# Kernel tuning notes

Hardware: AMD Instinct MI355X
Metric: run time of the kernel (lower is better)

Reference implementation:

```python
import jax, jax.numpy as jnp
import numpy as np

N_LAYER = 4
N_HEAD = 8
N_EMBD = 512
HEAD_SIZE = N_EMBD // N_HEAD
VOCAB = 32000
BLOCK = 2048
WINDOW = 64
N_GLOBAL = 16
N_RANDOM = 16
B = 2
T = 2048


def setup_inputs() -> dict:
    key = jax.random.key(0)
    ks = jax.random.split(key, 24)
    s = 0.02
    inp = {
        "tok_emb": jax.random.normal(ks[0], (VOCAB, N_EMBD), jnp.float32) * s,
        "pos_emb": jax.random.normal(ks[1], (BLOCK, N_EMBD), jnp.float32) * s,
        "Wq": jax.random.normal(ks[2], (N_LAYER, N_HEAD, N_EMBD, HEAD_SIZE), jnp.float32) * s,
        "Wk": jax.random.normal(ks[3], (N_LAYER, N_HEAD, N_EMBD, HEAD_SIZE), jnp.float32) * s,
        "Wv": jax.random.normal(ks[4], (N_LAYER, N_HEAD, N_EMBD, HEAD_SIZE), jnp.float32) * s,
        "Wproj": jax.random.normal(ks[5], (N_LAYER, N_EMBD, N_EMBD), jnp.float32) * s,
        "bproj": jnp.zeros((N_LAYER, N_EMBD), jnp.float32),
        "ln1_g": jnp.ones((N_LAYER, N_EMBD), jnp.float32),
        "ln1_b": jnp.zeros((N_LAYER, N_EMBD), jnp.float32),
        "ln2_g": jnp.ones((N_LAYER, N_EMBD), jnp.float32),
        "ln2_b": jnp.zeros((N_LAYER, N_EMBD), jnp.float32),
        "W1": jax.random.normal(ks[6], (N_LAYER, N_EMBD, 4 * N_EMBD), jnp.float32) * s,
        "b1": jnp.zeros((N_LAYER, 4 * N_EMBD), jnp.float32),
        "W2": jax.random.normal(ks[7], (N_LAYER, 4 * N_EMBD, N_EMBD), jnp.float32) * s,
        "b2": jnp.zeros((N_LAYER, N_EMBD), jnp.float32),
        "lnf_g": jnp.ones((N_EMBD,), jnp.float32),
        "lnf_b": jnp.zeros((N_EMBD,), jnp.float32),
        "Wout": jax.random.normal(ks[8], (N_EMBD, VOCAB), jnp.float32) * s,
        "bout": jnp.zeros((VOCAB,), jnp.float32),
        "input_tokens": jax.random.randint(ks[9], (B, T), 0, VOCAB, jnp.int32),
        "random_cols": jax.random.randint(ks[10], (N_LAYER, N_HEAD, T, N_RANDOM), 0, T, jnp.int32),
    }
    return inp


def _layernorm(x, g, b):
    mu = jnp.mean(x, axis=-1, keepdims=True)
    var = jnp.var(x, axis=-1, keepdims=True)
    return (x - mu) * jax.lax.rsqrt(var + 1e-5) * g + b


def _static_masks(t):
    rows = jnp.arange(t)[:, None]
    cols = jnp.arange(t)[None, :]
    causal = rows >= cols
    local = (cols >= rows - WINDOW + 1) & (cols <= rows)
    glob = (rows < N_GLOBAL) | (cols < N_GLOBAL)
    return local | glob, causal  # base [T,T], causal [T,T]


def _random_mask(rc):  # rc: [H, T, R] -> [H, T, T] bool
    h, t, r = rc.shape
    m = jnp.zeros((h, t, t), dtype=bool)
    hi = jnp.arange(h)[:, None, None]
    ri = jnp.arange(t)[None, :, None]
    return m.at[hi, ri, rc].set(True)


def _forward(tok_emb, pos_emb, Wq, Wk, Wv, Wproj, bproj, ln1_g, ln1_b, ln2_g, ln2_b,
             W1, b1, W2, b2, lnf_g, lnf_b, Wout, bout, input_tokens, random_cols):
    b, t = input_tokens.shape
    x = tok_emb[input_tokens] + pos_emb[:t]  # [B,T,C]
    base, causal = _static_masks(t)
    scale = HEAD_SIZE ** -0.5
    neg_inf = jnp.finfo(x.dtype).min
    for l in range(N_LAYER):
        xn = _layernorm(x, ln1_g[l], ln1_b[l])
        q = jnp.einsum('btc,hcd->bhtd', xn, Wq[l])
        k = jnp.einsum('btc,hcd->bhtd', xn, Wk[l])
        v = jnp.einsum('btc,hcd->bhtd', xn, Wv[l])
        w = jnp.einsum('bhtd,bhsd->bhts', q, k) * scale  # [B,H,T,T]
        final = (base[None] | _random_mask(random_cols[l])) & causal[None]  # [H,T,T]
        w = jnp.where(final[None], w, neg_inf)
        w = jax.nn.softmax(w, axis=-1)
        attn = jnp.einsum('bhts,bhsd->bhtd', w, v)  # [B,H,T,hs]
        attn = attn.transpose(0, 2, 1, 3).reshape(b, t, N_EMBD)
        x = x + attn @ Wproj[l] + bproj[l]
        xn = _layernorm(x, ln2_g[l], ln2_b[l])
        h = jax.nn.relu(xn @ W1[l] + b1[l])
        x = x + h @ W2[l] + b2[l]
    x = _layernorm(x, lnf_g, lnf_b)
    return x @ Wout + bout  # logits [B,T,V]


def reference(tok_emb, pos_emb, Wq, Wk, Wv, Wproj, bproj, ln1_g, ln1_b, ln2_g, ln2_b,
              W1, b1, W2, b2, lnf_g, lnf_b, Wout, bout, input_tokens, random_cols):
    return _forward(tok_emb, pos_emb, Wq, Wk, Wv, Wproj, bproj, ln1_g, ln1_b, ln2_g, ln2_b,
                    W1, b1, W2, b2, lnf_g, lnf_b, Wout, bout, input_tokens, random_cols)
```

## Files before the change

kernel.cpp:

```cpp
#include <hip/hip_runtime.h>
#include <hip/hip_bf16.h>

#define NLAYER 4
#define NHEAD 8
#define CEMB 512
#define HS 64
#define VOCAB_N 32000
#define SEQT 2048
#define BATCH_N 2
#define MROWS (BATCH_N * SEQT)
#define WIN 64
#define NGLOB 16
#define NRAND 16
#define QB 16

typedef __attribute__((ext_vector_type(8))) __bf16 bf16x8;
typedef __attribute__((ext_vector_type(4))) float f32x4;
typedef __attribute__((ext_vector_type(8))) unsigned short u16x8;

__device__ __forceinline__ unsigned short f2bf(float f) {
    unsigned u = __float_as_uint(f);
    u += 0x7fffu + ((u >> 16) & 1u);
    return (unsigned short)(u >> 16);
}
__device__ __forceinline__ float bf2f(unsigned short v) {
    return __uint_as_float((unsigned)v << 16);
}

__device__ __forceinline__ void stage16(const unsigned short* g, unsigned short* l) {
    __builtin_amdgcn_global_load_lds(
        (const __attribute__((address_space(1))) void*)g,
        (__attribute__((address_space(3))) void*)l, 16, 0, 0);
}

__global__ __launch_bounds__(256) void transpose_all_kernel(
    const float* __restrict__ Wq, const float* __restrict__ Wk,
    const float* __restrict__ Wv, const float* __restrict__ Wproj,
    const float* __restrict__ W1, const float* __restrict__ W2,
    const float* __restrict__ Wout,
    unsigned short* __restrict__ wqkvT, unsigned short* __restrict__ wprojT,
    unsigned short* __restrict__ w1T, unsigned short* __restrict__ w2T,
    unsigned short* __restrict__ woutT)
{
    __shared__ float tle[64][65];
    const int bid = blockIdx.x;
    const float* src; unsigned short* dst; int Ks, Ns, k0, n0;
    if (bid < 768) {
        const int tile = bid & 7, rest = bid >> 3;
        const int l = rest / 24, r2 = rest % 24;
        const int sel = r2 >> 3, h = r2 & 7;
        const float* W = (sel == 0) ? Wq : (sel == 1) ? Wk : Wv;
        src = W + (size_t)(l * 8 + h) * 512 * 64;
        dst = wqkvT + ((size_t)l * 1536 + sel * 512 + h * 64) * 512;
        Ks = 512; Ns = 64; k0 = tile * 64; n0 = 0;
    } else if (bid < 1024) {
        const int idx = bid - 768, l = idx >> 6, t6 = idx & 63;
        src = Wproj + (size_t)l * 512 * 512;
        dst = wprojT + (size_t)l * 512 * 512;
        Ks = 512; Ns = 512; k0 = (t6 >> 3) * 64; n0 = (t6 & 7) * 64;
    } else if (bid < 2048) {
        const int idx = bid - 1024, l = idx >> 8, t8 = idx & 255;
        src = W1 + (size_t)l * 512 * 2048;
        dst = w1T + (size_t)l * 2048 * 512;
        Ks = 512; Ns = 2048; k0 = (t8 >> 5) * 64; n0 = (t8 & 31) * 64;
    } else if (bid < 3072) {
        const int idx = bid - 2048, l = idx >> 8, t8 = idx & 255;
        src = W2 + (size_t)l * 2048 * 512;
        dst = w2T + (size_t)l * 512 * 2048;
        Ks = 2048; Ns = 512; k0 = (t8 >> 3) * 64; n0 = (t8 & 7) * 64;
    } else {
        const int idx = bid - 3072;
        src = Wout; dst = woutT;
        Ks = 512; Ns = 32000; k0 = (idx / 500) * 64; n0 = (idx % 500) * 64;
    }
    const int tid = threadIdx.x;
    #pragma unroll
    for (int i = 0; i < 16; ++i) {
        const int idx = tid + i * 256;
        const int r = idx >> 6, c = idx & 63;
        tle[r][c] = src[(size_t)(k0 + r) * Ns + n0 + c];
    }
    __syncthreads();
    #pragma unroll
    for (int i = 0; i < 16; ++i) {
        const int idx = tid + i * 256;
        const int c = idx >> 6, r = idx & 63;
        dst[(size_t)(n0 + c) * Ks + k0 + r] = f2bf(tle[r][c]);
    }
}

__global__ __launch_bounds__(256) void embed_kernel(
    const float* __restrict__ tok_emb, const float* __restrict__ pos_emb,
    const int* __restrict__ toks, float* __restrict__ x)
{
    int i = blockIdx.x * 256 + threadIdx.x;
    int m = i >> 7;
    int c = (i & 127) << 2;
    int tok = toks[m];
    const float4 a = *(const float4*)&tok_emb[(size_t)tok * CEMB + c];
    const float4 p = *(const float4*)&pos_emb[(size_t)(m & (SEQT - 1)) * CEMB + c];
    float4 o;
    o.x = a.x + p.x; o.y = a.y + p.y; o.z = a.z + p.z; o.w = a.w + p.w;
    *(float4*)&x[(size_t)m * CEMB + c] = o;
}

__global__ __launch_bounds__(256) void ln_kernel(
    const float* __restrict__ x, const float* __restrict__ g,
    const float* __restrict__ b, unsigned short* __restrict__ out)
{
    const int wave = threadIdx.x >> 6, lane = threadIdx.x & 63;
    const int m = blockIdx.x * 4 + wave;
    const float* row = x + (size_t)m * CEMB;
    const float4 v0 = *(const float4*)&row[lane * 8];
    const float4 v1 = *(const float4*)&row[lane * 8 + 4];
    float s  = v0.x + v0.y + v0.z + v0.w + v1.x + v1.y + v1.z + v1.w;
    float s2 = v0.x*v0.x + v0.y*v0.y + v0.z*v0.z + v0.w*v0.w
             + v1.x*v1.x + v1.y*v1.y + v1.z*v1.z + v1.w*v1.w;
    #pragma unroll
    for (int off = 32; off > 0; off >>= 1) {
        s  += __shfl_xor(s, off);
        s2 += __shfl_xor(s2, off);
    }
    const float mu  = s * (1.f / CEMB);
    const float var = s2 * (1.f / CEMB) - mu * mu;
    const float rs  = rsqrtf(var + 1e-5f);
    const float vals[8] = {v0.x, v0.y, v0.z, v0.w, v1.x, v1.y, v1.z, v1.w};
    u16x8 o;
    #pragma unroll
    for (int j = 0; j < 8; ++j)
        o[j] = f2bf((vals[j] - mu) * rs * g[lane * 8 + j] + b[lane * 8 + j]);
    *(u16x8*)&out[(size_t)m * CEMB + lane * 8] = o;
}

template<int MODE, int NF, int SWZ>
__global__ __launch_bounds__(256) void gemm_kernel(
    const unsigned short* __restrict__ A, const unsigned short* __restrict__ Bt,
    const float* __restrict__ bias, const float* resid, void* outp,
    int M, int N, int K)
{
    __shared__ unsigned short sa[3][128 * 32];
    __shared__ unsigned short sb[3][NF * 32 * 32];
    const int tid = threadIdx.x;
    const int lane = tid & 63;
    const int wave = tid >> 6;
    const int wr = wave >> 1, wc = wave & 1;

    int bx = blockIdx.x, by = blockIdx.y;
    if (SWZ == 2) {
        const int flat = by * gridDim.x + bx;
        const int q = (gridDim.x * gridDim.y) >> 3;
        const int nl = (flat & 7) * q + (flat >> 3);
        by = nl & 31;
        bx = nl >> 5;
    }
    const int m0 = by * 128;
    const int n0 = bx * (NF * 32);

    const int c0a = (wave * 2) * 64 + lane;
    const int c1a = (wave * 2 + 1) * 64 + lane;
    const int r0 = c0a >> 2, kk0 = (c0a & 3) * 8;
    const int r1 = c1a >> 2, kk1 = (c1a & 3) * 8;
    const unsigned short* ga0 = A + (size_t)(m0 + r0) * K + kk0;
    const unsigned short* ga1 = A + (size_t)(m0 + r1) * K + kk1;
    const int o0 = (wave * 2) * 512;
    const int o1 = (wave * 2 + 1) * 512;
    const int cb0 = (NF == 4) ? c0a : wave * 64 + lane;
    const int cb1 = c1a;
    const int rb0 = cb0 >> 2, kb0 = (cb0 & 3) * 8;
    const int rb1 = cb1 >> 2, kb1 = (cb1 & 3) * 8;
    const unsigned short* gb0 = Bt + (size_t)(n0 + rb0) * K + kb0;
    const unsigned short* gb1 = Bt + (size_t)(n0 + rb1) * K + kb1;
    const int ob0 = (NF == 4) ? o0 : wave * 512;
    const int ob1 = o1;

    f32x4 acc[4][NF] = {};
    const int kro = (lane >> 4) * 8;
    const int fr = lane & 15;

    auto STAGE = [&](int tile, int buf) {
        const int kk = tile << 5;
        stage16(ga0 + kk, &sa[buf][o0]);
        stage16(ga1 + kk, &sa[buf][o1]);
        stage16(gb0 + kk, &sb[buf][ob0]);
        if constexpr (NF == 4) stage16(gb1 + kk, &sb[buf][ob1]);
    };

    const int nt = K >> 5;
    STAGE(0, 0);
    STAGE(1, 1);

    int cur = 0;
    for (int t = 0; t < nt; ++t) {
        if (t + 1 < nt) {
            if constexpr (NF == 2) asm volatile("s_waitcnt vmcnt(3)" ::: "memory");
            else                   asm volatile("s_waitcnt vmcnt(4)" ::: "memory");
        } else {
            asm volatile("s_waitcnt vmcnt(0)" ::: "memory");
        }
        __builtin_amdgcn_s_barrier();
        __builtin_amdgcn_sched_barrier(0);

        if (t + 2 < nt) {
            int b2 = cur + 2; if (b2 >= 3) b2 -= 3;
            STAGE(t + 2, b2);
        }

        bf16x8 af[4], bfr[NF];
        #pragma unroll
        for (int i = 0; i < 4; ++i)
            af[i] = *reinterpret_cast<const bf16x8*>(&sa[cur][(wr * 64 + i * 16 + fr) * 32 + kro]);
        #pragma unroll
        for (int i = 0; i < NF; ++i)
            bfr[i] = *reinterpret_cast<const bf16x8*>(&sb[cur][(wc * (NF * 16) + i * 16 + fr) * 32 + kro]);
        #pragma unroll
        for (int mi = 0; mi < 4; ++mi)
            #pragma unroll
            for (int ni = 0; ni < NF; ++ni)
                acc[mi][ni] = __builtin_amdgcn_mfma_f32_16x16x32_bf16(af[mi], bfr[ni], acc[mi][ni], 0, 0, 0);

        cur = (cur == 2) ? 0 : cur + 1;
    }

    #pragma unroll
    for (int mi = 0; mi < 4; ++mi) {
        #pragma unroll
        for (int ni = 0; ni < NF; ++ni) {
            const int gc = n0 + wc * (NF * 16) + ni * 16 + fr;
            const float bv = (MODE != 0) ? bias[gc] : 0.f;
            #pragma unroll
            for (int r = 0; r < 4; ++r) {
                const int gr = m0 + wr * 64 + mi * 16 + (lane >> 4) * 4 + r;
                float v = acc[mi][ni][r] + bv;
                if (MODE == 1) v += resid[(size_t)gr * N + gc];
                if (MODE == 2) v = fmaxf(v, 0.f);
                if (MODE == 0 || MODE == 2) {
                    ((unsigned short*)outp)[(size_t)gr * N + gc] = f2bf(v);
                } else {
                    ((float*)outp)[(size_t)gr * N + gc] = v;
                }
            }
        }
    }
}

__global__ __launch_bounds__(256) void attn_kernel(
    const unsigned short* __restrict__ qkv, const int* __restrict__ rc,
    unsigned short* __restrict__ attnout)
{
    __shared__ unsigned short Kw[80 * 64];
    __shared__ unsigned short Vw[80 * 64];
    __shared__ float ewA[4][64];
    __shared__ float cwW[4][40];
    __shared__ int   cwC[4][40];

    const int tid = threadIdx.x;
    const int wave = tid >> 6, lane = tid & 63;
    const int bid = blockIdx.x;
    const int tb = bid & 127;
    const int h = (bid >> 7) & 7;
    const int b = bid >> 10;
    const int t0 = tb * QB;
    const int base = t0 - 63;

    const unsigned short* kb = qkv + (size_t)b * SEQT * 1536 + 512 + h * 64;
    const unsigned short* vb = qkv + (size_t)b * SEQT * 1536 + 1024 + h * 64;

    for (int c = tid; c < 79 * 8; c += 256) {
        const int r = c >> 3, j = c & 7;
        const int col = base + r;
        u16x8 kv = {0, 0, 0, 0, 0, 0, 0, 0};
        u16x8 vv = {0, 0, 0, 0, 0, 0, 0, 0};
        if (col >= 0) {
            kv = *(const u16x8*)&kb[(size_t)col * 1536 + j * 8];
            vv = *(const u16x8*)&vb[(size_t)col * 1536 + j * 8];
        }
        *(u16x8*)&Kw[r * 64 + ((j ^ (r & 7)) * 8)] = kv;
        *(u16x8*)&Vw[r * 64 + j * 8] = vv;
    }
    __syncthreads();

    for (int u = 0; u < 4; ++u) {
        const int Q = wave * 4 + u;
        const int t = t0 + Q;
        const int m = b * SEQT + t;

        u16x8 qreg[8];
        #pragma unroll
        for (int j = 0; j < 8; ++j)
            qreg[j] = *(const u16x8*)&qkv[(size_t)m * 1536 + h * 64 + j * 8];

        const int row = Q + lane;
        const int colA = base + row;
        float sA;
        {
            float s = 0.f;
            #pragma unroll
            for (int j = 0; j < 8; ++j) {
                const u16x8 kc = *(const u16x8*)&Kw[row * 64 + ((j ^ (row & 7)) * 8)];
                #pragma unroll
                for (int e = 0; e < 8; ++e)
                    s += bf2f(kc[e]) * bf2f(qreg[j][e]);
            }
            sA = (colA >= NGLOB) ? s * 0.125f : -1e30f;
        }

        int colB = 0;
        bool vB = false;
        if (lane < NGLOB) {
            colB = lane;
            vB = (lane <= t);
        } else if (lane < 32) {
            colB = rc[((size_t)h * SEQT + t) * NRAND + (lane - 16)];
            vB = (colB >= NGLOB) && (colB <= t - WIN);
        }
        #pragma unroll
        for (int j = 0; j < 15; ++j) {
            const int cj = __shfl(colB, 16 + j);
            if (lane >= 16 && lane < 32 && (lane - 16) > j && cj == colB) vB = false;
        }

        float sB = -1e30f;
        if (vB) {
            float s = 0.f;
            const unsigned short* kr = &kb[(size_t)colB * 1536];
            #pragma unroll
            for (int j = 0; j < 8; ++j) {
                const u16x8 kc = *(const u16x8*)&kr[j * 8];
                #pragma unroll
                for (int e = 0; e < 8; ++e)
                    s += bf2f(kc[e]) * bf2f(qreg[j][e]);
            }
            sB = s * 0.125f;
        }

        float mx = fmaxf(sA, sB);
        #pragma unroll
        for (int off = 32; off > 0; off >>= 1) mx = fmaxf(mx, __shfl_xor(mx, off));
        const float e0 = (colA >= NGLOB) ? __expf(sA - mx) : 0.f;
        const float e1 = vB ? __expf(sB - mx) : 0.f;
        float sum = e0 + e1;
        #pragma unroll
        for (int off = 32; off > 0; off >>= 1) sum += __shfl_xor(sum, off);
        const float inv = 1.f / sum;

        ewA[wave][lane] = e0;
        const unsigned long long bm = __ballot(vB);
        const int nB = __popcll(bm);
        const int pos = __popcll(bm & ((1ull << lane) - 1ull));
        if (vB) { cwC[wave][pos] = colB; cwW[wave][pos] = e1; }
        if (lane >= 32 && lane < 36) {
            const int p = nB + (lane - 32);
            cwC[wave][p] = 0; cwW[wave][p] = 0.f;
        }

        float acc = 0.f;
        #pragma unroll 8
        for (int s = 0; s < 64; ++s)
            acc += ewA[wave][s] * bf2f(Vw[(Q + s) * 64 + lane]);

        const int nB4 = (nB + 3) & ~3;
        for (int i = 0; i < nB4; i += 4) {
            const float w0 = cwW[wave][i + 0], w1 = cwW[wave][i + 1];
            const float w2 = cwW[wave][i + 2], w3 = cwW[wave][i + 3];
            const int   c0 = cwC[wave][i + 0], c1 = cwC[wave][i + 1];
            const int   c2 = cwC[wave][i + 2], c3 = cwC[wave][i + 3];
            const float x0 = bf2f(vb[(size_t)c0 * 1536 + lane]);
            const float x1 = bf2f(vb[(size_t)c1 * 1536 + lane]);
            const float x2 = bf2f(vb[(size_t)c2 * 1536 + lane]);
            const float x3 = bf2f(vb[(size_t)c3 * 1536 + lane]);
            acc += w0 * x0 + w1 * x1 + w2 * x2 + w3 * x3;
        }

        attnout[(size_t)m * CEMB + h * 64 + lane] = f2bf(acc * inv);
    }
}

extern "C" void kernel_launch(void* const* d_in, const int* in_sizes, int n_in,
                              void* d_out, int out_size, void* d_ws, size_t ws_size,
                              hipStream_t stream)
{
    const float* tok_emb = (const float*)d_in[0];
    const float* pos_emb = (const float*)d_in[1];
    const float* Wq    = (const float*)d_in[2];
    const float* Wk    = (const float*)d_in[3];
    const float* Wv    = (const float*)d_in[4];
    const float* Wproj = (const float*)d_in[5];
    const float* bproj = (const float*)d_in[6];
    const float* ln1g  = (const float*)d_in[7];
    const float* ln1b  = (const float*)d_in[8];
    const float* ln2g  = (const float*)d_in[9];
    const float* ln2b  = (const float*)d_in[10];
    const float* W1    = (const float*)d_in[11];
    const float* b1    = (const float*)d_in[12];
    const float* W2    = (const float*)d_in[13];
    const float* b2    = (const float*)d_in[14];
    const float* lnfg  = (const float*)d_in[15];
    const float* lnfb  = (const float*)d_in[16];
    const float* Wout  = (const float*)d_in[17];
    const float* bout  = (const float*)d_in[18];
    const int*   toks  = (const int*)d_in[19];
    const int*   rcols = (const int*)d_in[20];
    (void)in_sizes; (void)n_in; (void)out_size; (void)ws_size;

    char* ws = (char*)d_ws;
    size_t off = 0;
    auto ALLOC = [&](size_t bytes) -> void* {
        void* p = ws + off;
        off += (bytes + 255) & ~(size_t)255;
        return p;
    };
    float*          x      = (float*)ALLOC((size_t)MROWS * CEMB * 4);
    unsigned short* xnbf   = (unsigned short*)ALLOC((size_t)MROWS * CEMB * 2);
    unsigned short* qkv    = (unsigned short*)ALLOC((size_t)MROWS * 1536 * 2);
    unsigned short* attnbf = (unsigned short*)ALLOC((size_t)MROWS * CEMB * 2);
    unsigned short* hbf    = (unsigned short*)ALLOC((size_t)MROWS * 2048 * 2);
    unsigned short* wqkvT  = (unsigned short*)ALLOC((size_t)NLAYER * 1536 * 512 * 2);
    unsigned short* wprojT = (unsigned short*)ALLOC((size_t)NLAYER * 512 * 512 * 2);
    unsigned short* w1T    = (unsigned short*)ALLOC((size_t)NLAYER * 2048 * 512 * 2);
    unsigned short* w2T    = (unsigned short*)ALLOC((size_t)NLAYER * 512 * 2048 * 2);
    unsigned short* woutT  = (unsigned short*)ALLOC((size_t)VOCAB_N * 512 * 2);

    transpose_all_kernel<<<7072, 256, 0, stream>>>(
        Wq, Wk, Wv, Wproj, W1, W2, Wout, wqkvT, wprojT, w1T, w2T, woutT);

    embed_kernel<<<2048, 256, 0, stream>>>(tok_emb, pos_emb, toks, x);

    for (int l = 0; l < NLAYER; ++l) {
        ln_kernel<<<1024, 256, 0, stream>>>(x, ln1g + l * CEMB, ln1b + l * CEMB, xnbf);
        gemm_kernel<0, 2, 0><<<dim3(24, 32), 256, 0, stream>>>(
            xnbf, wqkvT + (size_t)l * 1536 * 512, nullptr, nullptr, qkv, MROWS, 1536, 512);
        attn_kernel<<<2048, 256, 0, stream>>>(qkv, rcols + (size_t)l * NHEAD * SEQT * NRAND, attnbf);
        gemm_kernel<1, 2, 0><<<dim3(8, 32), 256, 0, stream>>>(
            attnbf, wprojT + (size_t)l * 512 * 512, bproj + l * CEMB, x, x, MROWS, 512, 512);
        ln_kernel<<<1024, 256, 0, stream>>>(x, ln2g + l * CEMB, ln2b + l * CEMB, xnbf);
        gemm_kernel<2, 4, 0><<<dim3(16, 32), 256, 0, stream>>>(
            xnbf, w1T + (size_t)l * 2048 * 512, b1 + l * 2048, nullptr, hbf, MROWS, 2048, 512);
        gemm_kernel<1, 2, 0><<<dim3(8, 32), 256, 0, stream>>>(
            hbf, w2T + (size_t)l * 512 * 2048, b2 + l * CEMB, x, x, MROWS, 512, 2048);
    }
    ln_kernel<<<1024, 256, 0, stream>>>(x, lnfg, lnfb, xnbf);
    gemm_kernel<3, 4, 2><<<dim3(250, 32), 256, 0, stream>>>(
        xnbf, woutT, bout, nullptr, d_out, MROWS, VOCAB_N, 512);
}
```

Baseline: 1.035 ms.

## Rewrite sparse attention with MFMA for window scores and PV product

The attention kernel now has each wave handle 16 queries and computes the sliding-window plus global scores with bf16 16x16x32 MFMA tiles instead of per-lane scalar dot products. Probabilities are written to LDS as bf16 and multiplied against a transposed V tile (window plus global columns) with MFMA. Random columns are still handled with scalar gathers. Blocks now cover 64 queries, so the grid shrinks to 512 blocks. This aims to cut scalar FMA and LDS traffic, at the cost of rounding probabilities to bf16, more LDS per block, and fewer blocks in flight.

```diff
diff --git a/kernel.cpp b/kernel.cpp
--- a/kernel.cpp
+++ b/kernel.cpp
@@ -12,7 +12,6 @@
 #define WIN 64
 #define NGLOB 16
 #define NRAND 16
-#define QB 16
 
 typedef __attribute__((ext_vector_type(8))) __bf16 bf16x8;
 typedef __attribute__((ext_vector_type(4))) float f32x4;
@@ -25,6 +24,9 @@
 }
 __device__ __forceinline__ float bf2f(unsigned short v) {
     return __uint_as_float((unsigned)v << 16);
+}
+__device__ __forceinline__ bf16x8 asbf(u16x8 v) {
+    return __builtin_bit_cast(bf16x8, v);
 }
 
 __device__ __forceinline__ void stage16(const unsigned short* g, unsigned short* l) {
@@ -243,135 +245,217 @@
     }
 }
 
+#define VTS 168
+#define PSS 104
+#define OSS 68
 __global__ __launch_bounds__(256) void attn_kernel(
     const unsigned short* __restrict__ qkv, const int* __restrict__ rc,
     unsigned short* __restrict__ attnout)
 {
-    __shared__ unsigned short Kw[80 * 64];
-    __shared__ unsigned short Vw[80 * 64];
-    __shared__ float ewA[4][64];
-    __shared__ float cwW[4][40];
-    __shared__ int   cwC[4][40];
+    __shared__ unsigned short Vt[64 * VTS];
+    __shared__ unsigned short Ps[4][16 * PSS];
+    __shared__ float Osh[4][16 * OSS];
+    __shared__ unsigned short rWs[4][16][16];
+    __shared__ short rCs[4][16][16];
+    __shared__ float qmaxr[4][16];
+    __shared__ float qsumr[4][16];
+    __shared__ float qinvA[4][16];
 
     const int tid = threadIdx.x;
-    const int wave = tid >> 6, lane = tid & 63;
+    const int wv = tid >> 6, lane = tid & 63;
+    const int l15 = lane & 15, lq = lane >> 4;
     const int bid = blockIdx.x;
-    const int tb = bid & 127;
-    const int h = (bid >> 7) & 7;
-    const int b = bid >> 10;
-    const int t0 = tb * QB;
-    const int base = t0 - 63;
-
-    const unsigned short* kb = qkv + (size_t)b * SEQT * 1536 + 512 + h * 64;
-    const unsigned short* vb = qkv + (size_t)b * SEQT * 1536 + 1024 + h * 64;
-
-    for (int c = tid; c < 79 * 8; c += 256) {
-        const int r = c >> 3, j = c & 7;
-        const int col = base + r;
-        u16x8 kv = {0, 0, 0, 0, 0, 0, 0, 0};
-        u16x8 vv = {0, 0, 0, 0, 0, 0, 0, 0};
-        if (col >= 0) {
-            kv = *(const u16x8*)&kb[(size_t)col * 1536 + j * 8];
-            vv = *(const u16x8*)&vb[(size_t)col * 1536 + j * 8];
-        }
-        *(u16x8*)&Kw[r * 64 + ((j ^ (r & 7)) * 8)] = kv;
-        *(u16x8*)&Vw[r * 64 + j * 8] = vv;
-    }
-    __syncthreads();
-
-    for (int u = 0; u < 4; ++u) {
-        const int Q = wave * 4 + u;
-        const int t = t0 + Q;
-        const int m = b * SEQT + t;
-
-        u16x8 qreg[8];
-        #pragma unroll
-        for (int j = 0; j < 8; ++j)
-            qreg[j] = *(const u16x8*)&qkv[(size_t)m * 1536 + h * 64 + j * 8];
-
-        const int row = Q + lane;
-        const int colA = base + row;
-        float sA;
-        {
-            float s = 0.f;
+    const int tg = bid & 31;
+    const int h = (bid >> 5) & 7;
+    const int b = bid >> 8;
+    const int t0 = tg * 64;
+    const int tq0 = t0 + wv * 16;
+
+    const unsigned short* qb = qkv + (size_t)b * SEQT * 1536 + h * 64;
+    const unsigned short* kb = qb + 512;
+    const unsigned short* vb = qb + 1024;
+
+    for (int idx = tid; idx < 1152; idx += 256) {
+        const int j = idx / 144;
+        const int s = idx - j * 144;
+        int col = (s < 128) ? (t0 - 64 + s) : (s - 128);
+        if (col < 0) col = 0;
+        const u16x8 v = *(const u16x8*)&vb[(size_t)col * 1536 + j * 8];
+        #pragma unroll
+        for (int e = 0; e < 8; ++e)
+            Vt[(j * 8 + e) * VTS + s] = v[e];
+    }
+
+    const int qrow = tq0 + l15;
+    const u16x8 a0 = *(const u16x8*)&qb[(size_t)qrow * 1536 + lq * 8];
+    const u16x8 a1 = *(const u16x8*)&qb[(size_t)qrow * 1536 + 32 + lq * 8];
+
+    f32x4 sfr[6] = {};
+    #pragma unroll
+    for (int tile = 0; tile < 6; ++tile) {
+        int c = (tile < 5) ? (tq0 - 64 + tile * 16 + l15) : l15;
+        if (c < 0) c = 0;
+        const unsigned short* kr = &kb[(size_t)c * 1536 + lq * 8];
+        const u16x8 b0 = *(const u16x8*)&kr[0];
+        const u16x8 b1 = *(const u16x8*)&kr[32];
+        sfr[tile] = __builtin_amdgcn_mfma_f32_16x16x32_bf16(asbf(a0), asbf(b0), sfr[tile], 0, 0, 0);
+        sfr[tile] = __builtin_amdgcn_mfma_f32_16x16x32_bf16(asbf(a1), asbf(b1), sfr[tile], 0, 0, 0);
+    }
+
+    float sw[24];
+    float mxw[4] = {-1e30f, -1e30f, -1e30f, -1e30f};
+    #pragma unroll
+    for (int tile = 0; tile < 6; ++tile) {
+        #pragma unroll
+        for (int r = 0; r < 4; ++r) {
+            const int dq = lq * 4 + r;
+            float v = sfr[tile][r] * 0.125f;
+            bool ok;
+            if (tile < 5) {
+                const int j = tile * 16 + l15;
+                const int c = tq0 - 64 + j;
+                ok = (j >= dq + 1) && (j <= dq + 64) && (c >= NGLOB);
+            } else {
+                ok = (l15 <= tq0 + dq);
+            }
+            v = ok ? v : -1e30f;
+            sw[tile * 4 + r] = v;
+            mxw[r] = fmaxf(mxw[r], v);
+        }
+    }
+    #pragma unroll
+    for (int r = 0; r < 4; ++r)
+        #pragma unroll
+        for (int off = 1; off < 16; off <<= 1)
+            mxw[r] = fmaxf(mxw[r], __shfl_xor(mxw[r], off));
+
+    const int myq = lane >> 2;
+    const int tq = tq0 + myq;
+    u16x8 qr[8];
+    #pragma unroll
+    for (int j = 0; j < 8; ++j)
+        qr[j] = *(const u16x8*)&qb[(size_t)tq * 1536 + j * 8];
+
+    int mycol[4]; bool mval[4];
+    #pragma unroll
+    for (int i = 0; i < 4; ++i) {
+        const int slot = (lane & 3) + 4 * i;
+        const int c = rc[((size_t)h * SEQT + tq) * NRAND + slot];
+        mycol[i] = c;
+        mval[i] = (c >= NGLOB) && (c <= tq - WIN);
+    }
+    #pragma unroll
+    for (int k = 0; k < 4; ++k) {
+        #pragma unroll
+        for (int i2 = 0; i2 < 4; ++i2) {
+            const int oc = __shfl(mycol[i2], (lane & ~3) + k);
+            const int os = k + 4 * i2;
             #pragma unroll
-            for (int j = 0; j < 8; ++j) {
-                const u16x8 kc = *(const u16x8*)&Kw[row * 64 + ((j ^ (row & 7)) * 8)];
-                #pragma unroll
-                for (int e = 0; e < 8; ++e)
-                    s += bf2f(kc[e]) * bf2f(qreg[j][e]);
-            }
-            sA = (colA >= NGLOB) ? s * 0.125f : -1e30f;
-        }
-
-        int colB = 0;
-        bool vB = false;
-        if (lane < NGLOB) {
-            colB = lane;
-            vB = (lane <= t);
-        } else if (lane < 32) {
-            colB = rc[((size_t)h * SEQT + t) * NRAND + (lane - 16)];
-            vB = (colB >= NGLOB) && (colB <= t - WIN);
-        }
-        #pragma unroll
-        for (int j = 0; j < 15; ++j) {
-            const int cj = __shfl(colB, 16 + j);
-            if (lane >= 16 && lane < 32 && (lane - 16) > j && cj == colB) vB = false;
-        }
-
-        float sB = -1e30f;
-        if (vB) {
-            float s = 0.f;
-            const unsigned short* kr = &kb[(size_t)colB * 1536];
+            for (int i = 0; i < 4; ++i)
+                if (oc == mycol[i] && os < (lane & 3) + 4 * i) mval[i] = false;
+        }
+    }
+    float sraw[4];
+    #pragma unroll
+    for (int i = 0; i < 4; ++i) {
+        float s = -1e30f;
+        if (mval[i]) {
+            float d = 0.f;
+            const unsigned short* kr = &kb[(size_t)mycol[i] * 1536];
             #pragma unroll
             for (int j = 0; j < 8; ++j) {
                 const u16x8 kc = *(const u16x8*)&kr[j * 8];
                 #pragma unroll
                 for (int e = 0; e < 8; ++e)
-                    s += bf2f(kc[e]) * bf2f(qreg[j][e]);
+                    d += bf2f(kc[e]) * bf2f(qr[j][e]);
             }
-            sB = s * 0.125f;
-        }
-
-        float mx = fmaxf(sA, sB);
-        #pragma unroll
-        for (int off = 32; off > 0; off >>= 1) mx = fmaxf(mx, __shfl_xor(mx, off));
-        const float e0 = (colA >= NGLOB) ? __expf(sA - mx) : 0.f;
-        const float e1 = vB ? __expf(sB - mx) : 0.f;
-        float sum = e0 + e1;
-        #pragma unroll
-        for (int off = 32; off > 0; off >>= 1) sum += __shfl_xor(sum, off);
-        const float inv = 1.f / sum;
-
-        ewA[wave][lane] = e0;
-        const unsigned long long bm = __ballot(vB);
-        const int nB = __popcll(bm);
-        const int pos = __popcll(bm & ((1ull << lane) - 1ull));
-        if (vB) { cwC[wave][pos] = colB; cwW[wave][pos] = e1; }
-        if (lane >= 32 && lane < 36) {
-            const int p = nB + (lane - 32);
-            cwC[wave][p] = 0; cwW[wave][p] = 0.f;
-        }
-
-        float acc = 0.f;
-        #pragma unroll 8
-        for (int s = 0; s < 64; ++s)
-            acc += ewA[wave][s] * bf2f(Vw[(Q + s) * 64 + lane]);
-
-        const int nB4 = (nB + 3) & ~3;
-        for (int i = 0; i < nB4; i += 4) {
-            const float w0 = cwW[wave][i + 0], w1 = cwW[wave][i + 1];
-            const float w2 = cwW[wave][i + 2], w3 = cwW[wave][i + 3];
-            const int   c0 = cwC[wave][i + 0], c1 = cwC[wave][i + 1];
-            const int   c2 = cwC[wave][i + 2], c3 = cwC[wave][i + 3];
-            const float x0 = bf2f(vb[(size_t)c0 * 1536 + lane]);
-            const float x1 = bf2f(vb[(size_t)c1 * 1536 + lane]);
-            const float x2 = bf2f(vb[(size_t)c2 * 1536 + lane]);
-            const float x3 = bf2f(vb[(size_t)c3 * 1536 + lane]);
-            acc += w0 * x0 + w1 * x1 + w2 * x2 + w3 * x3;
-        }
-
-        attnout[(size_t)m * CEMB + h * 64 + lane] = f2bf(acc * inv);
+            s = d * 0.125f;
+        }
+        sraw[i] = s;
+    }
+    float m4 = fmaxf(fmaxf(sraw[0], sraw[1]), fmaxf(sraw[2], sraw[3]));
+    m4 = fmaxf(m4, __shfl_xor(m4, 1));
+    m4 = fmaxf(m4, __shfl_xor(m4, 2));
+    if ((lane & 3) == 0) qmaxr[wv][myq] = m4;
+
+    float mx[4];
+    #pragma unroll
+    for (int r = 0; r < 4; ++r) {
+        const float rm = qmaxr[wv][lq * 4 + r];
+        mx[r] = fmaxf(mxw[r], rm);
+        if (l15 == 0) qmaxr[wv][lq * 4 + r] = mx[r];
+    }
+
+    const float qm = qmaxr[wv][myq];
+    float s4 = 0.f;
+    float er[4];
+    #pragma unroll
+    for (int i = 0; i < 4; ++i) {
+        er[i] = mval[i] ? __expf(sraw[i] - qm) : 0.f;
+        s4 += er[i];
+    }
+    s4 += __shfl_xor(s4, 1);
+    s4 += __shfl_xor(s4, 2);
+    if ((lane & 3) == 0) qsumr[wv][myq] = s4;
+    #pragma unroll
+    for (int i = 0; i < 4; ++i) {
+        rWs[wv][myq][(lane & 3) + 4 * i] = f2bf(er[i]);
+        rCs[wv][myq][(lane & 3) + 4 * i] = (short)mycol[i];
+    }
+
+    #pragma unroll
+    for (int r = 0; r < 4; ++r) {
+        float sm = 0.f;
+        #pragma unroll
+        for (int tile = 0; tile < 6; ++tile) {
+            const float e = __expf(sw[tile * 4 + r] - mx[r]);
+            sw[tile * 4 + r] = e;
+            sm += e;
+        }
+        #pragma unroll
+        for (int off = 1; off < 16; off <<= 1) sm += __shfl_xor(sm, off);
+        const float tot = sm + qsumr[wv][lq * 4 + r];
+        const float iv = 1.f / tot;
+        if (l15 == 0) qinvA[wv][lq * 4 + r] = iv;
+    }
+    #pragma unroll
+    for (int tile = 0; tile < 6; ++tile)
+        #pragma unroll
+        for (int r = 0; r < 4; ++r)
+            Ps[wv][(lq * 4 + r) * PSS + tile * 16 + l15] = f2bf(sw[tile * 4 + r]);
+
+    __syncthreads();
+
+    f32x4 of[4] = {};
+    #pragma unroll
+    for (int kf = 0; kf < 3; ++kf) {
+        const bf16x8 af = *reinterpret_cast<const bf16x8*>(&Ps[wv][l15 * PSS + kf * 32 + lq * 8]);
+        const int ks0 = kf * 32 + lq * 8;
+        const int s0 = (ks0 < 80) ? (wv * 16 + ks0) : (ks0 + 48);
+        #pragma unroll
+        for (int nt = 0; nt < 4; ++nt) {
+            const bf16x8 bv = *reinterpret_cast<const bf16x8*>(&Vt[(nt * 16 + l15) * VTS + s0]);
+            of[nt] = __builtin_amdgcn_mfma_f32_16x16x32_bf16(af, bv, of[nt], 0, 0, 0);
+        }
+    }
+    #pragma unroll
+    for (int nt = 0; nt < 4; ++nt)
+        #pragma unroll
+        for (int r = 0; r < 4; ++r)
+            Osh[wv][(lq * 4 + r) * OSS + nt * 16 + l15] = of[nt][r];
+
+    for (int q = 0; q < 16; ++q) {
+        const int m = b * SEQT + tq0 + q;
+        float acc = Osh[wv][q * OSS + lane];
+        #pragma unroll 4
+        for (int s2 = 0; s2 < 16; ++s2) {
+            const float w = bf2f(rWs[wv][q][s2]);
+            if (w != 0.f) {
+                const int c = rCs[wv][q][s2];
+                acc += w * bf2f(vb[(size_t)c * 1536 + lane]);
+            }
+        }
+        attnout[(size_t)m * CEMB + h * 64 + lane] = f2bf(acc * qinvA[wv][q]);
     }
 }
 
@@ -429,7 +513,7 @@
         ln_kernel<<<1024, 256, 0, stream>>>(x, ln1g + l * CEMB, ln1b + l * CEMB, xnbf);
         gemm_kernel<0, 2, 0><<<dim3(24, 32), 256, 0, stream>>>(
             xnbf, wqkvT + (size_t)l * 1536 * 512, nullptr, nullptr, qkv, MROWS, 1536, 512);
-        attn_kernel<<<2048, 256, 0, stream>>>(qkv, rcols + (size_t)l * NHEAD * SEQT * NRAND, attnbf);
+        attn_kernel<<<512, 256, 0, stream>>>(qkv, rcols + (size_t)l * NHEAD * SEQT * NRAND, attnbf);
         gemm_kernel<1, 2, 0><<<dim3(8, 32), 256, 0, stream>>>(
             attnbf, wprojT + (size_t)l * 512 * 512, bproj + l * CEMB, x, x, MROWS, 512, 512);
         ln_kernel<<<1024, 256, 0, stream>>>(x, ln2g + l * CEMB, ln2b + l * CEMB, xnbf);
```

Measured after the change: 1.065 ms. 1.03x slower.

## Fuse layernorm into GEMM prologues using row stats from residual epilogues

Applied to the files above, without the earlier changes.

Drops the standalone layernorm kernels. The residual-add GEMM epilogues and the embed kernel now write per-row partial sums and sums of squares into a stats buffer. A new gemm_ln_kernel reduces those partials to mean and rstd, then loads fp32 activations and applies the normalization while converting A tiles to bf16 in shared memory. This removes the launches and the round trip through the bf16 normalized buffer, but every N-tile now redoes the fp32 load and normalize work, the fused GEMM drops to double buffering, and the swizzle is removed from the plain GEMM.

```diff
diff --git a/kernel.cpp b/kernel.cpp
--- a/kernel.cpp
+++ b/kernel.cpp
@@ -91,52 +91,47 @@
 
 __global__ __launch_bounds__(256) void embed_kernel(
     const float* __restrict__ tok_emb, const float* __restrict__ pos_emb,
-    const int* __restrict__ toks, float* __restrict__ x)
+    const int* __restrict__ toks, float* __restrict__ x,
+    float* __restrict__ statsA)
 {
-    int i = blockIdx.x * 256 + threadIdx.x;
-    int m = i >> 7;
-    int c = (i & 127) << 2;
-    int tok = toks[m];
+    __shared__ float ws[4], ws2[4];
+    const int tid = threadIdx.x;
+    const int i = blockIdx.x * 256 + tid;
+    const int m = i >> 7;
+    const int c = (i & 127) << 2;
+    const int wave = tid >> 6, lane = tid & 63;
+    const int tok = toks[m];
     const float4 a = *(const float4*)&tok_emb[(size_t)tok * CEMB + c];
     const float4 p = *(const float4*)&pos_emb[(size_t)(m & (SEQT - 1)) * CEMB + c];
     float4 o;
     o.x = a.x + p.x; o.y = a.y + p.y; o.z = a.z + p.z; o.w = a.w + p.w;
     *(float4*)&x[(size_t)m * CEMB + c] = o;
-}
-
-__global__ __launch_bounds__(256) void ln_kernel(
-    const float* __restrict__ x, const float* __restrict__ g,
-    const float* __restrict__ b, unsigned short* __restrict__ out)
-{
-    const int wave = threadIdx.x >> 6, lane = threadIdx.x & 63;
-    const int m = blockIdx.x * 4 + wave;
-    const float* row = x + (size_t)m * CEMB;
-    const float4 v0 = *(const float4*)&row[lane * 8];
-    const float4 v1 = *(const float4*)&row[lane * 8 + 4];
-    float s  = v0.x + v0.y + v0.z + v0.w + v1.x + v1.y + v1.z + v1.w;
-    float s2 = v0.x*v0.x + v0.y*v0.y + v0.z*v0.z + v0.w*v0.w
-             + v1.x*v1.x + v1.y*v1.y + v1.z*v1.z + v1.w*v1.w;
+    float s  = o.x + o.y + o.z + o.w;
+    float s2 = o.x*o.x + o.y*o.y + o.z*o.z + o.w*o.w;
     #pragma unroll
     for (int off = 32; off > 0; off >>= 1) {
         s  += __shfl_xor(s, off);
         s2 += __shfl_xor(s2, off);
     }
-    const float mu  = s * (1.f / CEMB);
-    const float var = s2 * (1.f / CEMB) - mu * mu;
-    const float rs  = rsqrtf(var + 1e-5f);
-    const float vals[8] = {v0.x, v0.y, v0.z, v0.w, v1.x, v1.y, v1.z, v1.w};
-    u16x8 o;
-    #pragma unroll
-    for (int j = 0; j < 8; ++j)
-        o[j] = f2bf((vals[j] - mu) * rs * g[lane * 8 + j] + b[lane * 8 + j]);
-    *(u16x8*)&out[(size_t)m * CEMB + lane * 8] = o;
-}
-
-template<int MODE, int NF, int SWZ>
+    if (lane == 0) { ws[wave] = s; ws2[wave] = s2; }
+    __syncthreads();
+    if (tid < 16) {
+        const int r = tid >> 3;
+        const int j = tid & 7;
+        float4 z = {0.f, 0.f, 0.f, 0.f};
+        if (j == 0) {
+            z.x = ws[2 * r] + ws[2 * r + 1];
+            z.y = ws2[2 * r] + ws2[2 * r + 1];
+        }
+        *(float4*)&statsA[(size_t)(blockIdx.x * 2 + r) * 32 + j * 4] = z;
+    }
+}
+
+template<int MODE, int NF, int STATS>
 __global__ __launch_bounds__(256) void gemm_kernel(
     const unsigned short* __restrict__ A, const unsigned short* __restrict__ Bt,
     const float* __restrict__ bias, const float* resid, void* outp,
-    int M, int N, int K)
+    float* __restrict__ statsOut, int M, int N, int K)
 {
     __shared__ unsigned short sa[3][128 * 32];
     __shared__ unsigned short sb[3][NF * 32 * 32];
@@ -144,15 +139,7 @@
     const int lane = tid & 63;
     const int wave = tid >> 6;
     const int wr = wave >> 1, wc = wave & 1;
-
-    int bx = blockIdx.x, by = blockIdx.y;
-    if (SWZ == 2) {
-        const int flat = by * gridDim.x + bx;
-        const int q = (gridDim.x * gridDim.y) >> 3;
-        const int nl = (flat & 7) * q + (flat >> 3);
-        by = nl & 31;
-        bx = nl >> 5;
-    }
+    const int bx = blockIdx.x, by = blockIdx.y;
     const int m0 = by * 128;
     const int n0 = bx * (NF * 32);
 
@@ -221,6 +208,174 @@
         cur = (cur == 2) ? 0 : cur + 1;
     }
 
+    if constexpr (MODE == 1 && STATS) {
+        #pragma unroll
+        for (int mi = 0; mi < 4; ++mi) {
+            #pragma unroll
+            for (int r = 0; r < 4; ++r) {
+                const int gr = m0 + wr * 64 + mi * 16 + (lane >> 4) * 4 + r;
+                float s = 0.f, s2 = 0.f;
+                #pragma unroll
+                for (int ni = 0; ni < NF; ++ni) {
+                    const int gc = n0 + wc * (NF * 16) + ni * 16 + fr;
+                    float v = acc[mi][ni][r] + bias[gc] + resid[(size_t)gr * N + gc];
+                    ((float*)outp)[(size_t)gr * N + gc] = v;
+                    s += v; s2 += v * v;
+                }
+                s  += __shfl_xor(s, 1);  s2 += __shfl_xor(s2, 1);
+                s  += __shfl_xor(s, 2);  s2 += __shfl_xor(s2, 2);
+                s  += __shfl_xor(s, 4);  s2 += __shfl_xor(s2, 4);
+                s  += __shfl_xor(s, 8);  s2 += __shfl_xor(s2, 8);
+                if (fr == 0) {
+                    float2 st = {s, s2};
+                    *(float2*)&statsOut[(size_t)gr * 32 + (bx * 2 + wc) * 2] = st;
+                }
+            }
+        }
+    } else {
+        #pragma unroll
+        for (int mi = 0; mi < 4; ++mi) {
+            #pragma unroll
+            for (int ni = 0; ni < NF; ++ni) {
+                const int gc = n0 + wc * (NF * 16) + ni * 16 + fr;
+                const float bv = bias[gc];
+                #pragma unroll
+                for (int r = 0; r < 4; ++r) {
+                    const int gr = m0 + wr * 64 + mi * 16 + (lane >> 4) * 4 + r;
+                    float v = acc[mi][ni][r] + bv;
+                    if (MODE == 1) v += resid[(size_t)gr * N + gc];
+                    if (MODE == 2) {
+                        v = fmaxf(v, 0.f);
+                        ((unsigned short*)outp)[(size_t)gr * N + gc] = f2bf(v);
+                    } else {
+                        ((float*)outp)[(size_t)gr * N + gc] = v;
+                    }
+                }
+            }
+        }
+    }
+}
+
+template<int MODE, int NF, int SWZ>
+__global__ __launch_bounds__(256) void gemm_ln_kernel(
+    const float* __restrict__ X, const float* __restrict__ stats,
+    const float* __restrict__ lng, const float* __restrict__ lnb,
+    const unsigned short* __restrict__ Bt,
+    const float* __restrict__ bias, void* outp,
+    int M, int N, int K)
+{
+    __shared__ unsigned short sa[2][128 * 32];
+    __shared__ unsigned short sb[2][NF * 32 * 32];
+    __shared__ float mu_s[128], rs_s[128];
+    __shared__ float gs[512], bs[512];
+
+    const int tid = threadIdx.x;
+    const int lane = tid & 63;
+    const int wave = tid >> 6;
+    const int wr = wave >> 1, wc = wave & 1;
+
+    int bx = blockIdx.x, by = blockIdx.y;
+    if (SWZ == 2) {
+        const int flat = by * gridDim.x + bx;
+        const int q = (gridDim.x * gridDim.y) >> 3;
+        const int nl = (flat & 7) * q + (flat >> 3);
+        by = nl & 31;
+        bx = nl >> 5;
+    }
+    const int m0 = by * 128;
+    const int n0 = bx * (NF * 32);
+
+    if (tid < 128) {
+        const float* sp = stats + (size_t)(m0 + tid) * 32;
+        float s = 0.f, s2 = 0.f;
+        #pragma unroll
+        for (int i = 0; i < 8; ++i) {
+            const float4 v = *(const float4*)&sp[i * 4];
+            s += v.x + v.z; s2 += v.y + v.w;
+        }
+        const float mu = s * (1.f / 512.f);
+        const float var = s2 * (1.f / 512.f) - mu * mu;
+        mu_s[tid] = mu;
+        rs_s[tid] = rsqrtf(var + 1e-5f);
+    }
+    gs[tid] = lng[tid]; gs[tid + 256] = lng[tid + 256];
+    bs[tid] = lnb[tid]; bs[tid + 256] = lnb[tid + 256];
+    __syncthreads();
+
+    const int c0a = (wave * 2) * 64 + lane;
+    const int c1a = (wave * 2 + 1) * 64 + lane;
+    const int r0 = c0a >> 2, kk0 = (c0a & 3) * 8;
+    const int r1 = c1a >> 2, kk1 = (c1a & 3) * 8;
+    const float* gx0 = X + (size_t)(m0 + r0) * K + kk0;
+    const float* gx1 = X + (size_t)(m0 + r1) * K + kk1;
+    const float mu0 = mu_s[r0], irs0 = rs_s[r0];
+    const float mu1 = mu_s[r1], irs1 = rs_s[r1];
+    const int cb0 = (NF == 4) ? c0a : wave * 64 + lane;
+    const int cb1 = c1a;
+    const int rb0 = cb0 >> 2, kb0 = (cb0 & 3) * 8;
+    const int rb1 = cb1 >> 2, kb1 = (cb1 & 3) * 8;
+    const unsigned short* gb0 = Bt + (size_t)(n0 + rb0) * K + kb0;
+    const unsigned short* gb1 = Bt + (size_t)(n0 + rb1) * K + kb1;
+    const int ob0 = (NF == 4) ? (wave * 2) * 512 : wave * 512;
+    const int ob1 = (wave * 2 + 1) * 512;
+
+    f32x4 acc[4][NF] = {};
+    const int kro = (lane >> 4) * 8;
+    const int fr = lane & 15;
+
+    float a0r[8], a1r[8];
+    auto LDA = [&](int t) {
+        const int kk = t << 5;
+        float4 p = *(const float4*)&gx0[kk];
+        float4 q = *(const float4*)&gx0[kk + 4];
+        a0r[0] = p.x; a0r[1] = p.y; a0r[2] = p.z; a0r[3] = p.w;
+        a0r[4] = q.x; a0r[5] = q.y; a0r[6] = q.z; a0r[7] = q.w;
+        p = *(const float4*)&gx1[kk];
+        q = *(const float4*)&gx1[kk + 4];
+        a1r[0] = p.x; a1r[1] = p.y; a1r[2] = p.z; a1r[3] = p.w;
+        a1r[4] = q.x; a1r[5] = q.y; a1r[6] = q.z; a1r[7] = q.w;
+    };
+    auto WRA = [&](int t, int buf) {
+        const int kk = t << 5;
+        u16x8 w;
+        #pragma unroll
+        for (int j = 0; j < 8; ++j)
+            w[j] = f2bf((a0r[j] - mu0) * irs0 * gs[kk + kk0 + j] + bs[kk + kk0 + j]);
+        *(u16x8*)&sa[buf][c0a * 8] = w;
+        #pragma unroll
+        for (int j = 0; j < 8; ++j)
+            w[j] = f2bf((a1r[j] - mu1) * irs1 * gs[kk + kk1 + j] + bs[kk + kk1 + j]);
+        *(u16x8*)&sa[buf][c1a * 8] = w;
+    };
+    auto STB = [&](int t, int buf) {
+        const int kk = t << 5;
+        stage16(gb0 + kk, &sb[buf][ob0]);
+        if constexpr (NF == 4) stage16(gb1 + kk, &sb[buf][ob1]);
+    };
+
+    const int nt = K >> 5;
+    LDA(0); STB(0, 0); WRA(0, 0);
+    __syncthreads();
+    int cur = 0;
+    for (int t = 0; t < nt; ++t) {
+        if (t + 1 < nt) { LDA(t + 1); STB(t + 1, cur ^ 1); }
+        bf16x8 af[4], bfr[NF];
+        #pragma unroll
+        for (int i = 0; i < 4; ++i)
+            af[i] = *reinterpret_cast<const bf16x8*>(&sa[cur][(wr * 64 + i * 16 + fr) * 32 + kro]);
+        #pragma unroll
+        for (int i = 0; i < NF; ++i)
+            bfr[i] = *reinterpret_cast<const bf16x8*>(&sb[cur][(wc * (NF * 16) + i * 16 + fr) * 32 + kro]);
+        #pragma unroll
+        for (int mi = 0; mi < 4; ++mi)
+            #pragma unroll
+            for (int ni = 0; ni < NF; ++ni)
+                acc[mi][ni] = __builtin_amdgcn_mfma_f32_16x16x32_bf16(af[mi], bfr[ni], acc[mi][ni], 0, 0, 0);
+        if (t + 1 < nt) WRA(t + 1, cur ^ 1);
+        __syncthreads();
+        cur ^= 1;
+    }
+
     #pragma unroll
     for (int mi = 0; mi < 4; ++mi) {
         #pragma unroll
@@ -231,9 +386,10 @@
             for (int r = 0; r < 4; ++r) {
                 const int gr = m0 + wr * 64 + mi * 16 + (lane >> 4) * 4 + r;
                 float v = acc[mi][ni][r] + bv;
-                if (MODE == 1) v += resid[(size_t)gr * N + gc];
-                if (MODE == 2) v = fmaxf(v, 0.f);
-                if (MODE == 0 || MODE == 2) {
+                if (MODE == 2) {
+                    v = fmaxf(v, 0.f);
+                    ((unsigned short*)outp)[(size_t)gr * N + gc] = f2bf(v);
+                } else if (MODE == 0) {
                     ((unsigned short*)outp)[(size_t)gr * N + gc] = f2bf(v);
                 } else {
                     ((float*)outp)[(size_t)gr * N + gc] = v;
@@ -410,10 +566,11 @@
         return p;
     };
     float*          x      = (float*)ALLOC((size_t)MROWS * CEMB * 4);
-    unsigned short* xnbf   = (unsigned short*)ALLOC((size_t)MROWS * CEMB * 2);
     unsigned short* qkv    = (unsigned short*)ALLOC((size_t)MROWS * 1536 * 2);
     unsigned short* attnbf = (unsigned short*)ALLOC((size_t)MROWS * CEMB * 2);
     unsigned short* hbf    = (unsigned short*)ALLOC((size_t)MROWS * 2048 * 2);
+    float*          statsA = (float*)ALLOC((size_t)MROWS * 32 * 4);
+    float*          statsB = (float*)ALLOC((size_t)MROWS * 32 * 4);
     unsigned short* wqkvT  = (unsigned short*)ALLOC((size_t)NLAYER * 1536 * 512 * 2);
     unsigned short* wprojT = (unsigned short*)ALLOC((size_t)NLAYER * 512 * 512 * 2);
     unsigned short* w1T    = (unsigned short*)ALLOC((size_t)NLAYER * 2048 * 512 * 2);
@@ -423,22 +580,21 @@
     transpose_all_kernel<<<7072, 256, 0, stream>>>(
         Wq, Wk, Wv, Wproj, W1, W2, Wout, wqkvT, wprojT, w1T, w2T, woutT);
 
-    embed_kernel<<<2048, 256, 0, stream>>>(tok_emb, pos_emb, toks, x);
+    embed_kernel<<<2048, 256, 0, stream>>>(tok_emb, pos_emb, toks, x, statsA);
 
     for (int l = 0; l < NLAYER; ++l) {
-        ln_kernel<<<1024, 256, 0, stream>>>(x, ln1g + l * CEMB, ln1b + l * CEMB, xnbf);
-        gemm_kernel<0, 2, 0><<<dim3(24, 32), 256, 0, stream>>>(
-            xnbf, wqkvT + (size_t)l * 1536 * 512, nullptr, nullptr, qkv, MROWS, 1536, 512);
+        gemm_ln_kernel<0, 2, 0><<<dim3(24, 32), 256, 0, stream>>>(
+            x, statsA, ln1g + l * CEMB, ln1b + l * CEMB,
+            wqkvT + (size_t)l * 1536 * 512, nullptr, qkv, MROWS, 1536, 512);
         attn_kernel<<<2048, 256, 0, stream>>>(qkv, rcols + (size_t)l * NHEAD * SEQT * NRAND, attnbf);
-        gemm_kernel<1, 2, 0><<<dim3(8, 32), 256, 0, stream>>>(
-            attnbf, wprojT + (size_t)l * 512 * 512, bproj + l * CEMB, x, x, MROWS, 512, 512);
-        ln_kernel<<<1024, 256, 0, stream>>>(x, ln2g + l * CEMB, ln2b + l * CEMB, xnbf);
-        gemm_kernel<2, 4, 0><<<dim3(16, 32), 256, 0, stream>>>(
-            xnbf, w1T + (size_t)l * 2048 * 512, b1 + l * 2048, nullptr, hbf, MROWS, 2048, 512);
-        gemm_kernel<1, 2, 0><<<dim3(8, 32), 256, 0, stream>>>(
-            hbf, w2T + (size_t)l * 512 * 2048, b2 + l * CEMB, x, x, MROWS, 512, 2048);
-    }
-    ln_kernel<<<1024, 256, 0, stream>>>(x, lnfg, lnfb, xnbf);
-    gemm_kernel<3, 4, 2><<<dim3(250, 32), 256, 0, stream>>>(
-        xnbf, woutT, bout, nullptr, d_out, MROWS, VOCAB_N, 512);
-}
+        gemm_kernel<1, 2, 1><<<dim3(8, 32), 256, 0, stream>>>(
+            attnbf, wprojT + (size_t)l * 512 * 512, bproj + l * CEMB, x, x, statsB, MROWS, 512, 512);
+        gemm_ln_kernel<2, 4, 0><<<dim3(16, 32), 256, 0, stream>>>(
+            x, statsB, ln2g + l * CEMB, ln2b + l * CEMB,
+            w1T + (size_t)l * 2048 * 512, b1 + l * 2048, hbf, MROWS, 2048, 512);
+        gemm_kernel<1, 2, 1><<<dim3(8, 32), 256, 0, stream>>>(
+            hbf, w2T + (size_t)l * 512 * 2048, b2 + l * CEMB, x, x, statsA, MROWS, 512, 2048);
+    }
+    gemm_ln_kernel<3, 4, 2><<<dim3(250, 32), 256, 0, stream>>>(
+        x, statsA, lnfg, lnfb, woutT, bout, d_out, MROWS, VOCAB_N, 512);
+}
```

Result: slower. 1.163 ms (+12.4%).

## Add dedicated 256x128-tile logits GEMM kernel with 512 threads

Applied to the files above, without the earlier changes.

Replaces the generic GEMM for the vocab projection with a specialized kernel that uses 512-thread blocks, 256x128 output tiles and double-buffered LDS staging, while keeping the XCD-aware block swizzle. Each wave still computes a 64x64 sub-tile, but the larger block tile raises reuse of A and B loads across waves and halves the number of blocks. The generic gemm_kernel loses its swizzle template parameter. The trade-off is higher LDS and register use per block and a pipeline that goes from three buffers to two.

```diff
diff --git a/kernel.cpp b/kernel.cpp
--- a/kernel.cpp
+++ b/kernel.cpp
@@ -132,7 +132,7 @@
     *(u16x8*)&out[(size_t)m * CEMB + lane * 8] = o;
 }
 
-template<int MODE, int NF, int SWZ>
+template<int MODE, int NF>
 __global__ __launch_bounds__(256) void gemm_kernel(
     const unsigned short* __restrict__ A, const unsigned short* __restrict__ Bt,
     const float* __restrict__ bias, const float* resid, void* outp,
@@ -144,17 +144,8 @@
     const int lane = tid & 63;
     const int wave = tid >> 6;
     const int wr = wave >> 1, wc = wave & 1;
-
-    int bx = blockIdx.x, by = blockIdx.y;
-    if (SWZ == 2) {
-        const int flat = by * gridDim.x + bx;
-        const int q = (gridDim.x * gridDim.y) >> 3;
-        const int nl = (flat & 7) * q + (flat >> 3);
-        by = nl & 31;
-        bx = nl >> 5;
-    }
-    const int m0 = by * 128;
-    const int n0 = bx * (NF * 32);
+    const int m0 = blockIdx.y * 128;
+    const int n0 = blockIdx.x * (NF * 32);
 
     const int c0a = (wave * 2) * 64 + lane;
     const int c1a = (wave * 2 + 1) * 64 + lane;
@@ -238,6 +229,87 @@
                 } else {
                     ((float*)outp)[(size_t)gr * N + gc] = v;
                 }
+            }
+        }
+    }
+}
+
+__global__ __launch_bounds__(512) void gemm_logits_kernel(
+    const unsigned short* __restrict__ A, const unsigned short* __restrict__ Bt,
+    const float* __restrict__ bias, float* __restrict__ outp,
+    int M, int N, int K)
+{
+    __shared__ unsigned short sa[2][256 * 32];
+    __shared__ unsigned short sb[2][128 * 32];
+    const int tid = threadIdx.x;
+    const int lane = tid & 63;
+    const int wave = tid >> 6;
+    const int wr = wave >> 1, wc = wave & 1;
+
+    const int flat = blockIdx.y * gridDim.x + blockIdx.x;
+    const int q = (gridDim.x * gridDim.y) >> 3;
+    const int nl = (flat & 7) * q + (flat >> 3);
+    const int by = nl & 15;
+    const int bx = nl >> 4;
+    const int m0 = by * 256;
+    const int n0 = bx * 128;
+
+    const int c0a = (wave * 2) * 64 + lane;
+    const int c1a = (wave * 2 + 1) * 64 + lane;
+    const int r0 = c0a >> 2, kk0 = (c0a & 3) * 8;
+    const int r1 = c1a >> 2, kk1 = (c1a & 3) * 8;
+    const unsigned short* ga0 = A + (size_t)(m0 + r0) * K + kk0;
+    const unsigned short* ga1 = A + (size_t)(m0 + r1) * K + kk1;
+    const int o0 = (wave * 2) * 512;
+    const int o1 = (wave * 2 + 1) * 512;
+    const int cb0 = wave * 64 + lane;
+    const int rb0 = cb0 >> 2, kb0 = (cb0 & 3) * 8;
+    const unsigned short* gb0 = Bt + (size_t)(n0 + rb0) * K + kb0;
+    const int ob0 = wave * 512;
+
+    f32x4 acc[4][4] = {};
+    const int kro = (lane >> 4) * 8;
+    const int fr = lane & 15;
+
+    auto STAGE = [&](int t, int buf) {
+        const int kk = t << 5;
+        stage16(ga0 + kk, &sa[buf][o0]);
+        stage16(ga1 + kk, &sa[buf][o1]);
+        stage16(gb0 + kk, &sb[buf][ob0]);
+    };
+
+    const int nt = K >> 5;
+    STAGE(0, 0);
+    __syncthreads();
+    int cur = 0;
+    for (int t = 0; t < nt; ++t) {
+        if (t + 1 < nt) STAGE(t + 1, cur ^ 1);
+        bf16x8 af[4], bfr[4];
+        #pragma unroll
+        for (int i = 0; i < 4; ++i)
+            af[i] = *reinterpret_cast<const bf16x8*>(&sa[cur][(wr * 64 + i * 16 + fr) * 32 + kro]);
+        #pragma unroll
+        for (int i = 0; i < 4; ++i)
+            bfr[i] = *reinterpret_cast<const bf16x8*>(&sb[cur][(wc * 64 + i * 16 + fr) * 32 + kro]);
+        #pragma unroll
+        for (int mi = 0; mi < 4; ++mi)
+            #pragma unroll
+            for (int ni = 0; ni < 4; ++ni)
+                acc[mi][ni] = __builtin_amdgcn_mfma_f32_16x16x32_bf16(af[mi], bfr[ni], acc[mi][ni], 0, 0, 0);
+        __syncthreads();
+        cur ^= 1;
+    }
+
+    #pragma unroll
+    for (int mi = 0; mi < 4; ++mi) {
+        #pragma unroll
+        for (int ni = 0; ni < 4; ++ni) {
+            const int gc = n0 + wc * 64 + ni * 16 + fr;
+            const float bv = bias[gc];
+            #pragma unroll
+            for (int r = 0; r < 4; ++r) {
+                const int gr = m0 + wr * 64 + mi * 16 + (lane >> 4) * 4 + r;
+                outp[(size_t)gr * N + gc] = acc[mi][ni][r] + bv;
             }
         }
     }
@@ -427,18 +499,18 @@
 
     for (int l = 0; l < NLAYER; ++l) {
         ln_kernel<<<1024, 256, 0, stream>>>(x, ln1g + l * CEMB, ln1b + l * CEMB, xnbf);
-        gemm_kernel<0, 2, 0><<<dim3(24, 32), 256, 0, stream>>>(
+        gemm_kernel<0, 2><<<dim3(24, 32), 256, 0, stream>>>(
             xnbf, wqkvT + (size_t)l * 1536 * 512, nullptr, nullptr, qkv, MROWS, 1536, 512);
         attn_kernel<<<2048, 256, 0, stream>>>(qkv, rcols + (size_t)l * NHEAD * SEQT * NRAND, attnbf);
-        gemm_kernel<1, 2, 0><<<dim3(8, 32), 256, 0, stream>>>(
+        gemm_kernel<1, 2><<<dim3(8, 32), 256, 0, stream>>>(
             attnbf, wprojT + (size_t)l * 512 * 512, bproj + l * CEMB, x, x, MROWS, 512, 512);
         ln_kernel<<<1024, 256, 0, stream>>>(x, ln2g + l * CEMB, ln2b + l * CEMB, xnbf);
-        gemm_kernel<2, 4, 0><<<dim3(16, 32), 256, 0, stream>>>(
+        gemm_kernel<2, 4><<<dim3(16, 32), 256, 0, stream>>>(
             xnbf, w1T + (size_t)l * 2048 * 512, b1 + l * 2048, nullptr, hbf, MROWS, 2048, 512);
-        gemm_kernel<1, 2, 0><<<dim3(8, 32), 256, 0, stream>>>(
+        gemm_kernel<1, 2><<<dim3(8, 32), 256, 0, stream>>>(
             hbf, w2T + (size_t)l * 512 * 2048, b2 + l * CEMB, x, x, MROWS, 512, 2048);
     }
     ln_kernel<<<1024, 256, 0, stream>>>(x, lnfg, lnfb, xnbf);
-    gemm_kernel<3, 4, 2><<<dim3(250, 32), 256, 0, stream>>>(
-        xnbf, woutT, bout, nullptr, d_out, MROWS, VOCAB_N, 512);
-}
+    gemm_logits_kernel<<<dim3(250, 16), 512, 0, stream>>>(
+        xnbf, woutT, bout, (float*)d_out, MROWS, VOCAB_N, 512);
+}
```

Measured after the change: 1.027 ms. No clear change (-0.8%).
